# Kernel tuning notes

Hardware: AMD Instinct MI355X
Metric: run time of the kernel (lower is better)

## Reference

```python
import jax, jax.numpy as jnp
import numpy as np

B, S, D, V = 32, 1024, 768, 32000


def setup_inputs() -> dict:
    key = jax.random.key(0)
    ks = jax.random.split(key, 12)
    scale = 0.02
    return {
        "tokens": jax.random.randint(ks[0], (B, S), 0, V, dtype=jnp.int32),
        "mask": jax.random.randint(ks[1], (B, S), 0, 2, dtype=jnp.int32),
        "emb": jax.random.normal(ks[2], (V, D), dtype=jnp.float32) * scale,
        "wq": jax.random.normal(ks[3], (D, D), dtype=jnp.float32) * scale,
        "wk": jax.random.normal(ks[4], (D, D), dtype=jnp.float32) * scale,
        "wv": jax.random.normal(ks[5], (D, D), dtype=jnp.float32) * scale,
        "ln_g": jnp.ones((D,), dtype=jnp.float32),
        "ln_b": jnp.zeros((D,), dtype=jnp.float32),
        "w1": jax.random.normal(ks[6], (D, D), dtype=jnp.float32) * scale,
        "b1": jnp.zeros((D,), dtype=jnp.float32),
        "wh": jax.random.normal(ks[7], (D, 2), dtype=jnp.float32) * scale,
        "bh": jnp.zeros((2,), dtype=jnp.float32),
    }


def reference(tokens, mask, emb, wq, wk, wv, ln_g, ln_b, w1, b1, wh, bh):
    # embedding lookup: [B,S,D]
    x = emb[tokens]
    q = x @ wq
    k = x @ wk
    v = x @ wv
    # unscaled attention scores: [B,S,S]
    s = jnp.einsum("bsd,btd->bst", q, k)
    # additive padding mask (mask==1 -> -1e9), broadcast over query dim
    s = s + (-1e9) * mask.astype(s.dtype)[:, None, :]
    a = jax.nn.softmax(s, axis=-1)
    o = jnp.einsum("bst,btd->bsd", a, v)
    # classify on first token
    cls = o[:, 0, :]  # [B,D]
    mu = jnp.mean(cls, axis=-1, keepdims=True)
    var = jnp.var(cls, axis=-1, keepdims=True)
    h = (cls - mu) * jax.lax.rsqrt(var + 1e-5) * ln_g + ln_b
    h = jax.nn.gelu(h @ w1 + b1, approximate=False)
    logits = h @ wh + bh  # [B,2]
    return (logits, a)
```

## Files before the change

kernel.cpp:

```cpp
#include <hip/hip_runtime.h>
#include <hip/hip_bf16.h>

#define NB 32
#define SS 1024
#define DD 768

typedef __attribute__((ext_vector_type(8))) short bf16x8;
typedef __attribute__((ext_vector_type(4))) float f32x4;

__device__ inline ushort f2bf(float f) {
    union { float f; unsigned u; } x;
    x.f = f;
    unsigned r = (x.u + 0x7fffu + ((x.u >> 16) & 1u)) >> 16;
    return (ushort)r;
}

#define GLOBAL_PTR(x) ((const __attribute__((address_space(1))) void*)(x))
#define LDS_PTR(x)    ((__attribute__((address_space(3))) void*)(x))

__global__ void k_cvt(const float* __restrict__ wq, const float* __restrict__ wk,
                      ushort* __restrict__ wqb, ushort* __restrict__ wkb) {
    const int i = (blockIdx.x * 256 + threadIdx.x) * 4;
    const float* src = blockIdx.y ? wk : wq;
    ushort* dst = blockIdx.y ? wkb : wqb;
    const float4 v = *(const float4*)(src + i);
    ushort4 o;
    o.x = f2bf(v.x); o.y = f2bf(v.y); o.z = f2bf(v.z); o.w = f2bf(v.w);
    *(ushort4*)(dst + i) = o;
}

__global__ void k_gather(const int* __restrict__ tokens, const float* __restrict__ emb,
                         ushort* __restrict__ xb) {
    int i = (blockIdx.x * 256 + threadIdx.x) * 4;
    int row = i / DD;
    int col = i - row * DD;
    int tok = tokens[row];
    const float4 v = *(const float4*)(emb + (size_t)tok * DD + col);
    ushort4 o;
    o.x = f2bf(v.x); o.y = f2bf(v.y); o.z = f2bf(v.z); o.w = f2bf(v.w);
    *(ushort4*)(xb + (size_t)row * DD + col) = o;
}

__global__ __launch_bounds__(256, 2) void k_gemm_s(const ushort* __restrict__ A,
                                                   const ushort* __restrict__ Bt,
                                                   ushort* __restrict__ Cb) {
    constexpr int BK = 64;
    __shared__ ushort As[2][128 * BK];
    __shared__ ushort Bs[2][128 * BK];
    const int tid = threadIdx.x;
    const int wave = tid >> 6, lane = tid & 63;
    const int bx = blockIdx.x, by = blockIdx.y;
    const size_t abase = (size_t)bx * 128 * DD;
    const size_t bbase = (size_t)by * 128 * DD;
    const int r = tid >> 3;
    const int cc = (tid & 7) * 8;

    auto stage = [&](int buf, int k0) {
#pragma unroll
        for (int i = 0; i < 4; i++) {
            __builtin_amdgcn_global_load_lds(GLOBAL_PTR(A + abase + (size_t)(r + i * 32) * DD + k0 + cc),
                                             LDS_PTR(&As[buf][(r + i * 32) * BK + cc]), 16, 0, 0);
            __builtin_amdgcn_global_load_lds(GLOBAL_PTR(Bt + bbase + (size_t)(r + i * 32) * DD + k0 + cc),
                                             LDS_PTR(&Bs[buf][(r + i * 32) * BK + cc]), 16, 0, 0);
        }
    };

    f32x4 acc[4][4] = {};
    const int wm = (wave >> 1) * 64, wn = (wave & 1) * 64;
    const int lr = lane & 15, lc = (lane >> 4) * 8;

    stage(0, 0);
    __syncthreads();
    int cur = 0;
#pragma unroll 1
    for (int k0 = 0; k0 < DD; k0 += BK) {
        if (k0 + BK < DD) stage(cur ^ 1, k0 + BK);
        const ushort* as = As[cur];
        const ushort* bs = Bs[cur];
#pragma unroll
        for (int kk = 0; kk < 2; kk++) {
            bf16x8 af[4], bfv[4];
#pragma unroll
            for (int m = 0; m < 4; m++)
                af[m] = *(const bf16x8*)(as + (wm + m * 16 + lr) * BK + kk * 32 + lc);
#pragma unroll
            for (int n = 0; n < 4; n++)
                bfv[n] = *(const bf16x8*)(bs + (wn + n * 16 + lr) * BK + kk * 32 + lc);
#pragma unroll
            for (int m = 0; m < 4; m++)
#pragma unroll
                for (int n = 0; n < 4; n++)
                    acc[m][n] = __builtin_amdgcn_mfma_f32_16x16x32_bf16(af[m], bfv[n], acc[m][n], 0, 0, 0);
        }
        __syncthreads();
        cur ^= 1;
    }
    const int rowbase = bx * 128 + wm + (lane >> 4) * 4;
    const int colbase = by * 128 + wn + (lane & 15);
#pragma unroll
    for (int m = 0; m < 4; m++)
#pragma unroll
        for (int n = 0; n < 4; n++)
#pragma unroll
            for (int j = 0; j < 4; j++)
                Cb[(size_t)(rowbase + m * 16 + j) * DD + colbase + n * 16] = f2bf(acc[m][n][j]);
}

#define HALF_USH (128 * 64)
template <int MODE>
__global__ __launch_bounds__(512, 2) void k_gemm256(const ushort* __restrict__ A,
                                                    const ushort* __restrict__ Bt,
                                                    ushort* __restrict__ Cb,
                                                    float* __restrict__ Cs) {
    __shared__ ushort As[2][2][HALF_USH];
    __shared__ ushort Bs[2][2][HALF_USH];
    const int tid = threadIdx.x;
    const int wid = tid >> 6, lane = tid & 63;
    const int wm = wid >> 2, wn = wid & 3;
    const int la = lane & 15;

    int bx, by;
    size_t abase, bbase;
    if (MODE == 1) {
        const int wgid = blockIdx.x;
        const int g = wgid >> 7, w = wgid & 127;
        const int b = g * 8 + (w & 7);
        const int tile = w >> 3;
        bx = tile & 3; by = tile >> 2;
        abase = (size_t)b * SS * DD + (size_t)bx * 256 * DD;
        bbase = (size_t)b * SS * DD + (size_t)by * 256 * DD;
        Cs += (size_t)b * SS * SS;
    } else {
        bx = blockIdx.x; by = blockIdx.y;
        abase = (size_t)bx * 256 * DD;
        bbase = (size_t)by * 256 * DD;
    }
    const ushort* Ag = A + abase;
    const ushort* Bg = Bt + bbase;

    int s_r[2], s_c[2], s_d[2];
#pragma unroll
    for (int l = 0; l < 2; l++) {
        const int L = (l * 512 + tid) * 16;
        const int r = L >> 7;
        const int cb = L & 127;
        s_r[l] = r;
        s_c[l] = (cb ^ ((r & 7) << 4)) >> 1;
        s_d[l] = L >> 1;
    }

    auto stage_half = [&](ushort* dst, const ushort* gsrc) {
#pragma unroll
        for (int l = 0; l < 2; l++)
            __builtin_amdgcn_global_load_lds(GLOBAL_PTR(gsrc + (size_t)s_r[l] * DD + s_c[l]),
                                             LDS_PTR(dst + s_d[l]), 16, 0, 0);
    };

    const int swz = (la & 7) << 4;
    const int off_k0 = (((lane >> 4) << 4) ^ swz) >> 1;
    const int off_k1 = ((64 | ((lane >> 4) << 4)) ^ swz) >> 1;

    f32x4 acc[8][4] = {};

    stage_half(&As[0][0][0], Ag);
    stage_half(&As[0][1][0], Ag + (size_t)128 * DD);
    stage_half(&Bs[0][0][0], Bg);
    stage_half(&Bs[0][1][0], Bg + (size_t)128 * DD);
    __syncthreads();

#pragma unroll 1
    for (int t = 0; t < 12; t++) {
        const int buf = t & 1;
        const ushort* Ah = &As[buf][wm][0];
        const ushort* Bh = &Bs[buf][wn >> 1][0];
        const int brow0 = (wn & 1) * 64;
        const int kt = (t + 1) * 64;
        bf16x8 bfv[4][2];
#pragma unroll
        for (int q = 0; q < 4; q++) {
            if (q == 0) {
#pragma unroll
                for (int n = 0; n < 4; n++) {
                    const int rr = brow0 + n * 16 + la;
                    bfv[n][0] = *(const bf16x8*)(Bh + rr * 64 + off_k0);
                    bfv[n][1] = *(const bf16x8*)(Bh + rr * 64 + off_k1);
                }
            }
            bf16x8 af[2][2];
#pragma unroll
            for (int dm = 0; dm < 2; dm++) {
                const int rr = (q * 2 + dm) * 16 + la;
                af[dm][0] = *(const bf16x8*)(Ah + rr * 64 + off_k0);
                af[dm][1] = *(const bf16x8*)(Ah + rr * 64 + off_k1);
            }
            if (t < 11) {
                if (q == 0) stage_half(&As[buf ^ 1][0][0], Ag + kt);
                if (q == 1) stage_half(&As[buf ^ 1][1][0], Ag + (size_t)128 * DD + kt);
                if (q == 2) stage_half(&Bs[buf ^ 1][0][0], Bg + kt);
                if (q == 3) stage_half(&Bs[buf ^ 1][1][0], Bg + (size_t)128 * DD + kt);
            }
            __builtin_amdgcn_s_setprio(1);
#pragma unroll
            for (int dm = 0; dm < 2; dm++)
#pragma unroll
                for (int n = 0; n < 4; n++)
#pragma unroll
                    for (int kk = 0; kk < 2; kk++)
                        acc[q * 2 + dm][n] = __builtin_amdgcn_mfma_f32_16x16x32_bf16(
                            af[dm][kk], bfv[n][kk], acc[q * 2 + dm][n], 0, 0, 0);
            __builtin_amdgcn_s_setprio(0);
            if (q < 3) __builtin_amdgcn_s_barrier();
        }
        __syncthreads();
    }

    const int rowbase = bx * 256 + wm * 128 + (lane >> 4) * 4;
    const int colbase = by * 256 + wn * 64 + la;
    if (MODE == 0) {
#pragma unroll
        for (int m = 0; m < 8; m++)
#pragma unroll
            for (int n = 0; n < 4; n++)
#pragma unroll
                for (int j = 0; j < 4; j++)
                    Cb[(size_t)(rowbase + m * 16 + j) * DD + colbase + n * 16] = f2bf(acc[m][n][j]);
    } else {
#pragma unroll
        for (int m = 0; m < 8; m++)
#pragma unroll
            for (int n = 0; n < 4; n++)
#pragma unroll
                for (int j = 0; j < 4; j++)
                    Cs[(size_t)(rowbase + m * 16 + j) * SS + colbase + n * 16] = acc[m][n][j];
    }
}

__global__ __launch_bounds__(256) void k_softmax(float* __restrict__ a, const int* __restrict__ mask) {
    const int rid = blockIdx.x;
    const int b = rid >> 10, rr = rid & 1023;
    float* row = a + (size_t)b * SS * SS + (size_t)rr * SS;
    const int* mrow = mask + b * SS;
    const int t = threadIdx.x * 4;
    float4 v = *(float4*)(row + t);
    const int4 mk = *(const int4*)(mrow + t);
    float x0 = v.x + (mk.x ? -1e9f : 0.0f);
    float x1 = v.y + (mk.y ? -1e9f : 0.0f);
    float x2 = v.z + (mk.z ? -1e9f : 0.0f);
    float x3 = v.w + (mk.w ? -1e9f : 0.0f);
    float mx = fmaxf(fmaxf(x0, x1), fmaxf(x2, x3));
#pragma unroll
    for (int off = 32; off; off >>= 1) mx = fmaxf(mx, __shfl_xor(mx, off));
    __shared__ float redm[4], reds[4];
    if ((threadIdx.x & 63) == 0) redm[threadIdx.x >> 6] = mx;
    __syncthreads();
    mx = fmaxf(fmaxf(redm[0], redm[1]), fmaxf(redm[2], redm[3]));
    float e0 = expf(x0 - mx), e1 = expf(x1 - mx), e2 = expf(x2 - mx), e3 = expf(x3 - mx);
    float sm = e0 + e1 + e2 + e3;
#pragma unroll
    for (int off = 32; off; off >>= 1) sm += __shfl_xor(sm, off);
    if ((threadIdx.x & 63) == 0) reds[threadIdx.x >> 6] = sm;
    __syncthreads();
    sm = reds[0] + reds[1] + reds[2] + reds[3];
    const float inv = 1.0f / sm;
    v.x = e0 * inv; v.y = e1 * inv; v.z = e2 * inv; v.w = e3 * inv;
    *(float4*)(row + t) = v;
}

__global__ __launch_bounds__(256) void k_xbar(const float* __restrict__ a, const int* __restrict__ tokens,
                                              const float* __restrict__ emb, float* __restrict__ part) {
    const int b = blockIdx.x >> 3, c = blockIdx.x & 7;
    __shared__ float a0s[128];
    __shared__ int toks[128];
    const int tid = threadIdx.x;
    if (tid < 128) {
        a0s[tid] = a[(size_t)b * SS * SS + c * 128 + tid];
        toks[tid] = tokens[b * SS + c * 128 + tid];
    }
    __syncthreads();
    float acc0 = 0.f, acc1 = 0.f, acc2 = 0.f;
#pragma unroll 4
    for (int t = 0; t < 128; t++) {
        const float at = a0s[t];
        const float* er = emb + (size_t)toks[t] * DD;
        acc0 = fmaf(at, er[tid], acc0);
        acc1 = fmaf(at, er[tid + 256], acc1);
        acc2 = fmaf(at, er[tid + 512], acc2);
    }
    float* p = part + ((size_t)c * NB + b) * DD;
    p[tid] = acc0; p[tid + 256] = acc1; p[tid + 512] = acc2;
}

__global__ __launch_bounds__(128) void k_cls(const float* __restrict__ part, const float* __restrict__ wv,
                                             float* __restrict__ cls) {
    const int b = blockIdx.y, tid = threadIdx.x;
    const int c = blockIdx.x * 128 + tid;
    __shared__ float xb[DD];
#pragma unroll
    for (int j = 0; j < 6; j++) {
        const int k = tid + j * 128;
        float s = 0.f;
#pragma unroll
        for (int p = 0; p < 8; p++) s += part[((size_t)p * NB + b) * DD + k];
        xb[k] = s;
    }
    __syncthreads();
    float acc = 0.f;
#pragma unroll 8
    for (int k = 0; k < DD; k++) acc = fmaf(xb[k], wv[(size_t)k * DD + c], acc);
    cls[(size_t)b * DD + c] = acc;
}

__device__ inline float block_sum256(float v, float* red, int tid) {
#pragma unroll
    for (int off = 32; off; off >>= 1) v += __shfl_xor(v, off);
    __syncthreads();
    if ((tid & 63) == 0) red[tid >> 6] = v;
    __syncthreads();
    return red[0] + red[1] + red[2] + red[3];
}

__global__ __launch_bounds__(256) void k_ln(const float* __restrict__ cls, const float* __restrict__ ln_g,
                                            const float* __restrict__ ln_b, float* __restrict__ hs) {
    const int b = blockIdx.x, tid = threadIdx.x;
    __shared__ float red[4];
    float v[3];
#pragma unroll
    for (int j = 0; j < 3; j++) v[j] = cls[(size_t)b * DD + tid + j * 256];
    const float mu = block_sum256(v[0] + v[1] + v[2], red, tid) * (1.0f / DD);
    float dv = 0.f;
#pragma unroll
    for (int j = 0; j < 3; j++) { const float d = v[j] - mu; dv += d * d; }
    __syncthreads();
    const float var = block_sum256(dv, red, tid) * (1.0f / DD);
    const float sc = 1.0f / sqrtf(var + 1e-5f);
#pragma unroll
    for (int j = 0; j < 3; j++) {
        const int d = tid + j * 256;
        hs[(size_t)b * DD + d] = (v[j] - mu) * sc * ln_g[d] + ln_b[d];
    }
}

__global__ __launch_bounds__(128) void k_mlp(const float* __restrict__ hs, const float* __restrict__ w1,
                                             const float* __restrict__ b1, const float* __restrict__ wh,
                                             float* __restrict__ part_l) {
    const int b = blockIdx.y, tid = threadIdx.x;
    const int j = blockIdx.x * 128 + tid;
    __shared__ float h[DD];
#pragma unroll
    for (int q = 0; q < 6; q++) h[tid + q * 128] = hs[(size_t)b * DD + tid + q * 128];
    __syncthreads();
    float p = b1[j];
#pragma unroll 8
    for (int d = 0; d < DD; d++) p = fmaf(h[d], w1[(size_t)d * DD + j], p);
    const float g = 0.5f * p * (1.0f + erff(p * 0.70710678118654752f));
    float l0 = g * wh[j * 2 + 0];
    float l1 = g * wh[j * 2 + 1];
#pragma unroll
    for (int off = 32; off; off >>= 1) { l0 += __shfl_xor(l0, off); l1 += __shfl_xor(l1, off); }
    __shared__ float r0[2], r1[2];
    if ((tid & 63) == 0) { r0[tid >> 6] = l0; r1[tid >> 6] = l1; }
    __syncthreads();
    if (tid == 0) {
        part_l[((size_t)b * 6 + blockIdx.x) * 2 + 0] = r0[0] + r0[1];
        part_l[((size_t)b * 6 + blockIdx.x) * 2 + 1] = r1[0] + r1[1];
    }
}

__global__ __launch_bounds__(64) void k_final(const float* __restrict__ part_l, const float* __restrict__ bh,
                                              float* __restrict__ out) {
    const int b = threadIdx.x;
    if (b < NB) {
        float l0 = bh[0], l1 = bh[1];
#pragma unroll
        for (int c = 0; c < 6; c++) {
            l0 += part_l[((size_t)b * 6 + c) * 2 + 0];
            l1 += part_l[((size_t)b * 6 + c) * 2 + 1];
        }
        out[b * 2 + 0] = l0;
        out[b * 2 + 1] = l1;
    }
}

extern "C" void kernel_launch(void* const* d_in, const int* in_sizes, int n_in,
                              void* d_out, int out_size, void* d_ws, size_t ws_size,
                              hipStream_t stream) {
    const int*   tokens = (const int*)d_in[0];
    const int*   mask   = (const int*)d_in[1];
    const float* emb    = (const float*)d_in[2];
    const float* wq     = (const float*)d_in[3];
    const float* wk     = (const float*)d_in[4];
    const float* wv     = (const float*)d_in[5];
    const float* ln_g   = (const float*)d_in[6];
    const float* ln_b   = (const float*)d_in[7];
    const float* w1     = (const float*)d_in[8];
    const float* b1     = (const float*)d_in[9];
    const float* wh     = (const float*)d_in[10];
    const float* bh     = (const float*)d_in[11];
    float* out = (float*)d_out;

    char* ws = (char*)d_ws;
    const size_t XB = (size_t)NB * SS * DD * 2;
    const size_t WB = (size_t)DD * DD * 2;
    ushort* xb  = (ushort*)ws;
    ushort* yb  = (ushort*)(ws + XB);
    ushort* wqb = (ushort*)(ws + 2 * XB);
    ushort* wkb = (ushort*)(ws + 2 * XB + WB);
    ushort* Wt  = (ushort*)(ws + 2 * XB + 2 * WB);
    char*   p4  = ws + 2 * XB + 3 * WB;
    float*  part   = (float*)p4;
    float*  cls    = (float*)(p4 + 786432);
    float*  hsb    = (float*)(p4 + 786432 + 98304);
    float*  part_l = (float*)(p4 + 786432 + 2 * 98304);

    float* s_region = out + 64;

    k_cvt<<<dim3(576, 2), 256, 0, stream>>>(wq, wk, wqb, wkb);
    k_gather<<<24576, 256, 0, stream>>>(tokens, emb, xb);
    k_gemm_s<<<dim3(6, 6), 256, 0, stream>>>(wkb, wqb, Wt);
    k_gemm256<0><<<dim3(128, 3), 512, 0, stream>>>(xb, Wt, yb, nullptr);
    k_gemm256<1><<<512, 512, 0, stream>>>(yb, xb, nullptr, s_region);
    k_softmax<<<32768, 256, 0, stream>>>(s_region, mask);
    k_xbar<<<256, 256, 0, stream>>>(s_region, tokens, emb, part);
    k_cls<<<dim3(6, NB), 128, 0, stream>>>(part, wv, cls);
    k_ln<<<NB, 256, 0, stream>>>(cls, ln_g, ln_b, hsb);
    k_mlp<<<dim3(6, NB), 128, 0, stream>>>(hsb, w1, b1, wh, part_l);
    k_final<<<1, 64, 0, stream>>>(part_l, bh, out);
}
```

Before: 337.5 us.

## Fuse score GEMM with masked softmax into a single attention kernel

Replaces the separate score GEMM (which wrote raw fp32 scores to the output) and the row-wise softmax kernel with one kernel. Each workgroup computes a full 64x1024 row block of scores in registers, applies the mask, and does the max and sum reductions through cross-lane shuffles and LDS. It then writes the normalized probabilities once. This removes a full fp32 read-and-write pass over the 128 MB attention matrix, but it uses a single-buffered, unpipelined K loop with a large LDS footprint (about 140 KB per block), which may limit occupancy and the overlap of loads with compute.

```diff
diff --git a/kernel.cpp b/kernel.cpp
--- a/kernel.cpp
+++ b/kernel.cpp
@@ -107,11 +107,9 @@
 }
 
 #define HALF_USH (128 * 64)
-template <int MODE>
 __global__ __launch_bounds__(512, 2) void k_gemm256(const ushort* __restrict__ A,
                                                     const ushort* __restrict__ Bt,
-                                                    ushort* __restrict__ Cb,
-                                                    float* __restrict__ Cs) {
+                                                    ushort* __restrict__ Cb) {
     __shared__ ushort As[2][2][HALF_USH];
     __shared__ ushort Bs[2][2][HALF_USH];
     const int tid = threadIdx.x;
@@ -119,24 +117,9 @@
     const int wm = wid >> 2, wn = wid & 3;
     const int la = lane & 15;
 
-    int bx, by;
-    size_t abase, bbase;
-    if (MODE == 1) {
-        const int wgid = blockIdx.x;
-        const int g = wgid >> 7, w = wgid & 127;
-        const int b = g * 8 + (w & 7);
-        const int tile = w >> 3;
-        bx = tile & 3; by = tile >> 2;
-        abase = (size_t)b * SS * DD + (size_t)bx * 256 * DD;
-        bbase = (size_t)b * SS * DD + (size_t)by * 256 * DD;
-        Cs += (size_t)b * SS * SS;
-    } else {
-        bx = blockIdx.x; by = blockIdx.y;
-        abase = (size_t)bx * 256 * DD;
-        bbase = (size_t)by * 256 * DD;
-    }
-    const ushort* Ag = A + abase;
-    const ushort* Bg = Bt + bbase;
+    const int bx = blockIdx.x, by = blockIdx.y;
+    const ushort* Ag = A + (size_t)bx * 256 * DD;
+    const ushort* Bg = Bt + (size_t)by * 256 * DD;
 
     int s_r[2], s_c[2], s_d[2];
 #pragma unroll
@@ -216,54 +199,159 @@
 
     const int rowbase = bx * 256 + wm * 128 + (lane >> 4) * 4;
     const int colbase = by * 256 + wn * 64 + la;
-    if (MODE == 0) {
-#pragma unroll
-        for (int m = 0; m < 8; m++)
-#pragma unroll
-            for (int n = 0; n < 4; n++)
-#pragma unroll
-                for (int j = 0; j < 4; j++)
-                    Cb[(size_t)(rowbase + m * 16 + j) * DD + colbase + n * 16] = f2bf(acc[m][n][j]);
-    } else {
-#pragma unroll
-        for (int m = 0; m < 8; m++)
-#pragma unroll
-            for (int n = 0; n < 4; n++)
-#pragma unroll
-                for (int j = 0; j < 4; j++)
-                    Cs[(size_t)(rowbase + m * 16 + j) * SS + colbase + n * 16] = acc[m][n][j];
-    }
-}
-
-__global__ __launch_bounds__(256) void k_softmax(float* __restrict__ a, const int* __restrict__ mask) {
-    const int rid = blockIdx.x;
-    const int b = rid >> 10, rr = rid & 1023;
-    float* row = a + (size_t)b * SS * SS + (size_t)rr * SS;
-    const int* mrow = mask + b * SS;
-    const int t = threadIdx.x * 4;
-    float4 v = *(float4*)(row + t);
-    const int4 mk = *(const int4*)(mrow + t);
-    float x0 = v.x + (mk.x ? -1e9f : 0.0f);
-    float x1 = v.y + (mk.y ? -1e9f : 0.0f);
-    float x2 = v.z + (mk.z ? -1e9f : 0.0f);
-    float x3 = v.w + (mk.w ? -1e9f : 0.0f);
-    float mx = fmaxf(fmaxf(x0, x1), fmaxf(x2, x3));
-#pragma unroll
-    for (int off = 32; off; off >>= 1) mx = fmaxf(mx, __shfl_xor(mx, off));
-    __shared__ float redm[4], reds[4];
-    if ((threadIdx.x & 63) == 0) redm[threadIdx.x >> 6] = mx;
-    __syncthreads();
-    mx = fmaxf(fmaxf(redm[0], redm[1]), fmaxf(redm[2], redm[3]));
-    float e0 = expf(x0 - mx), e1 = expf(x1 - mx), e2 = expf(x2 - mx), e3 = expf(x3 - mx);
-    float sm = e0 + e1 + e2 + e3;
-#pragma unroll
-    for (int off = 32; off; off >>= 1) sm += __shfl_xor(sm, off);
-    if ((threadIdx.x & 63) == 0) reds[threadIdx.x >> 6] = sm;
-    __syncthreads();
-    sm = reds[0] + reds[1] + reds[2] + reds[3];
-    const float inv = 1.0f / sm;
-    v.x = e0 * inv; v.y = e1 * inv; v.z = e2 * inv; v.w = e3 * inv;
-    *(float4*)(row + t) = v;
+#pragma unroll
+    for (int m = 0; m < 8; m++)
+#pragma unroll
+        for (int n = 0; n < 4; n++)
+#pragma unroll
+            for (int j = 0; j < 4; j++)
+                Cb[(size_t)(rowbase + m * 16 + j) * DD + colbase + n * 16] = f2bf(acc[m][n][j]);
+}
+
+__global__ __launch_bounds__(512, 2) void k_attn(const ushort* __restrict__ Y,
+                                                 const ushort* __restrict__ X,
+                                                 const int* __restrict__ mask,
+                                                 float* __restrict__ Aout) {
+    __shared__ ushort Bsh[SS * 64];
+    __shared__ ushort Ash[64 * 64];
+    __shared__ int    Msk[SS];
+    __shared__ float  RedM[8][64];
+    __shared__ float  RedS[8][64];
+
+    const int tid = threadIdx.x;
+    const int wid = tid >> 6, lane = tid & 63;
+    const int la = lane & 15, lg = lane >> 4;
+
+    const int wgid = blockIdx.x;
+    const int g = wgid >> 7, w = wgid & 127;
+    const int b = g * 8 + (w & 7);
+    const int bx = w >> 3;
+    const ushort* Ag = Y + (size_t)b * SS * DD + (size_t)bx * 64 * DD;
+    const ushort* Bg = X + (size_t)b * SS * DD;
+    float* Ao = Aout + (size_t)b * SS * SS + (size_t)bx * 64 * SS;
+
+    Msk[tid] = mask[b * SS + tid];
+    Msk[tid + 512] = mask[b * SS + tid + 512];
+
+    const int r0 = tid >> 3;
+    const int cb0 = (tid & 7) << 4;
+    const int sc = (cb0 ^ ((r0 & 7) << 4)) >> 1;
+    const int dofs = tid * 8;
+
+    const int swz = (la & 7) << 4;
+    const int off_k0 = ((lg << 4) ^ swz) >> 1;
+    const int off_k1 = ((64 | (lg << 4)) ^ swz) >> 1;
+
+    f32x4 acc[4][8] = {};
+
+#pragma unroll 1
+    for (int t = 0; t < 12; t++) {
+        const int k0 = t * 64;
+        __syncthreads();
+        __builtin_amdgcn_global_load_lds(GLOBAL_PTR(Ag + (size_t)r0 * DD + k0 + sc),
+                                         LDS_PTR(Ash + dofs), 16, 0, 0);
+#pragma unroll
+        for (int l = 0; l < 16; l++)
+            __builtin_amdgcn_global_load_lds(GLOBAL_PTR(Bg + (size_t)(l * 64 + r0) * DD + k0 + sc),
+                                             LDS_PTR(Bsh + l * 4096 + dofs), 16, 0, 0);
+        __syncthreads();
+
+        bf16x8 af[4][2];
+#pragma unroll
+        for (int m = 0; m < 4; m++) {
+            const int rr = m * 16 + la;
+            af[m][0] = *(const bf16x8*)(Ash + rr * 64 + off_k0);
+            af[m][1] = *(const bf16x8*)(Ash + rr * 64 + off_k1);
+        }
+#pragma unroll
+        for (int n = 0; n < 8; n++) {
+            const int rr = wid * 128 + n * 16 + la;
+            bf16x8 bf0 = *(const bf16x8*)(Bsh + rr * 64 + off_k0);
+            bf16x8 bf1 = *(const bf16x8*)(Bsh + rr * 64 + off_k1);
+            __builtin_amdgcn_s_setprio(1);
+#pragma unroll
+            for (int m = 0; m < 4; m++) {
+                acc[m][n] = __builtin_amdgcn_mfma_f32_16x16x32_bf16(af[m][0], bf0, acc[m][n], 0, 0, 0);
+                acc[m][n] = __builtin_amdgcn_mfma_f32_16x16x32_bf16(af[m][1], bf1, acc[m][n], 0, 0, 0);
+            }
+            __builtin_amdgcn_s_setprio(0);
+        }
+    }
+    __syncthreads();
+
+    float bias[8];
+#pragma unroll
+    for (int n = 0; n < 8; n++)
+        bias[n] = Msk[wid * 128 + n * 16 + la] ? -1e9f : 0.0f;
+
+    float mxl[4][4];
+#pragma unroll
+    for (int m = 0; m < 4; m++)
+#pragma unroll
+        for (int j = 0; j < 4; j++) {
+            float v = -3.4e38f;
+#pragma unroll
+            for (int n = 0; n < 8; n++) v = fmaxf(v, acc[m][n][j] + bias[n]);
+#pragma unroll
+            for (int off = 1; off < 16; off <<= 1) v = fmaxf(v, __shfl_xor(v, off));
+            mxl[m][j] = v;
+        }
+    if (la == 0) {
+#pragma unroll
+        for (int m = 0; m < 4; m++)
+#pragma unroll
+            for (int j = 0; j < 4; j++)
+                RedM[wid][m * 16 + lg * 4 + j] = mxl[m][j];
+    }
+    __syncthreads();
+#pragma unroll
+    for (int m = 0; m < 4; m++)
+#pragma unroll
+        for (int j = 0; j < 4; j++) {
+            const int r = m * 16 + lg * 4 + j;
+            float v = RedM[0][r];
+#pragma unroll
+            for (int ww = 1; ww < 8; ww++) v = fmaxf(v, RedM[ww][r]);
+            mxl[m][j] = v;
+        }
+
+    float sml[4][4];
+#pragma unroll
+    for (int m = 0; m < 4; m++)
+#pragma unroll
+        for (int j = 0; j < 4; j++) {
+            float s = 0.f;
+#pragma unroll
+            for (int n = 0; n < 8; n++) {
+                const float e = __expf(acc[m][n][j] + bias[n] - mxl[m][j]);
+                acc[m][n][j] = e;
+                s += e;
+            }
+#pragma unroll
+            for (int off = 1; off < 16; off <<= 1) s += __shfl_xor(s, off);
+            sml[m][j] = s;
+        }
+    if (la == 0) {
+#pragma unroll
+        for (int m = 0; m < 4; m++)
+#pragma unroll
+            for (int j = 0; j < 4; j++)
+                RedS[wid][m * 16 + lg * 4 + j] = sml[m][j];
+    }
+    __syncthreads();
+#pragma unroll
+    for (int m = 0; m < 4; m++)
+#pragma unroll
+        for (int j = 0; j < 4; j++) {
+            const int r = m * 16 + lg * 4 + j;
+            float s = RedS[0][r];
+#pragma unroll
+            for (int ww = 1; ww < 8; ww++) s += RedS[ww][r];
+            const float inv = 1.0f / s;
+#pragma unroll
+            for (int n = 0; n < 8; n++)
+                Ao[(size_t)r * SS + wid * 128 + n * 16 + la] = acc[m][n][j] * inv;
+        }
 }
 
 __global__ __launch_bounds__(256) void k_xbar(const float* __restrict__ a, const int* __restrict__ tokens,
@@ -412,15 +500,14 @@
     float*  hsb    = (float*)(p4 + 786432 + 98304);
     float*  part_l = (float*)(p4 + 786432 + 2 * 98304);
 
-    float* s_region = out + 64;
+    float* a_region = out + 64;
 
     k_cvt<<<dim3(576, 2), 256, 0, stream>>>(wq, wk, wqb, wkb);
     k_gather<<<24576, 256, 0, stream>>>(tokens, emb, xb);
     k_gemm_s<<<dim3(6, 6), 256, 0, stream>>>(wkb, wqb, Wt);
-    k_gemm256<0><<<dim3(128, 3), 512, 0, stream>>>(xb, Wt, yb, nullptr);
-    k_gemm256<1><<<512, 512, 0, stream>>>(yb, xb, nullptr, s_region);
-    k_softmax<<<32768, 256, 0, stream>>>(s_region, mask);
-    k_xbar<<<256, 256, 0, stream>>>(s_region, tokens, emb, part);
+    k_gemm256<<<dim3(128, 3), 512, 0, stream>>>(xb, Wt, yb);
+    k_attn<<<512, 512, 0, stream>>>(yb, xb, mask, a_region);
+    k_xbar<<<256, 256, 0, stream>>>(a_region, tokens, emb, part);
     k_cls<<<dim3(6, NB), 128, 0, stream>>>(part, wv, cls);
     k_ln<<<NB, 256, 0, stream>>>(cls, ln_g, ln_b, hsb);
     k_mlp<<<dim3(6, NB), 128, 0, stream>>>(hsb, w1, b1, wh, part_l);
```

After: 319.0 us. -5.5%, faster.
